# Kernel tuning notes

Hardware: AMD Instinct MI355X
Metric: run time of the kernel (lower is better)

Reference implementation:

```python
import jax, jax.numpy as jnp
import numpy as np

D_MODEL = 1024
N_HEADS = 16
HEAD_DIM = D_MODEL // N_HEADS
WINDOW = 256


def setup_inputs() -> dict:
    key = jax.random.key(0)
    ks = jax.random.split(key, 5)
    s = 1.0 / np.sqrt(D_MODEL)
    x = jax.random.normal(ks[0], (1, 4096, D_MODEL), dtype=jnp.float32)
    W_qkv = jax.random.uniform(ks[1], (D_MODEL, 3 * D_MODEL), jnp.float32, -s, s)
    b_qkv = jax.random.uniform(ks[2], (3 * D_MODEL,), jnp.float32, -s, s)
    W_proj = jax.random.uniform(ks[3], (D_MODEL, D_MODEL), jnp.float32, -s, s)
    b_proj = jax.random.uniform(ks[4], (D_MODEL,), jnp.float32, -s, s)
    return {"x": x, "W_qkv": W_qkv, "b_qkv": b_qkv, "W_proj": W_proj, "b_proj": b_proj}


def reference(x, W_qkv, b_qkv, W_proj, b_proj):
    b, t, c = x.shape
    qkv = x @ W_qkv + b_qkv  # [b,t,3c]
    q, k, v = jnp.split(qkv, 3, axis=-1)
    # [b,h,t,d]
    q = q.reshape(b, t, N_HEADS, HEAD_DIM).transpose(0, 2, 1, 3)
    k = k.reshape(b, t, N_HEADS, HEAD_DIM).transpose(0, 2, 1, 3)
    v = v.reshape(b, t, N_HEADS, HEAD_DIM).transpose(0, 2, 1, 3)
    att = jnp.einsum('bhqd,bhkd->bhqk', q, k) / np.sqrt(HEAD_DIM)
    idx = jnp.arange(t)
    diff = idx[:, None] - idx[None, :]  # query - key
    allowed = (diff >= 0) & (diff < WINDOW)  # causal & local window
    att = jnp.where(allowed[None, None], att, -jnp.inf)
    att = jax.nn.softmax(att, axis=-1)
    y = jnp.einsum('bhqk,bhkd->bhqd', att, v)
    y = y.transpose(0, 2, 1, 3).reshape(b, t, c)
    return y @ W_proj + b_proj
```

## Files before the change

### kernel.cpp

```cpp
#include <hip/hip_runtime.h>
#include <stdint.h>

#define TSEQ 4096
#define DMODEL 1024
#define N3 3072
#define NHEADS 16
#define HDIM 64
#define WINDOW 256

typedef __attribute__((ext_vector_type(8))) short short8;
typedef __attribute__((ext_vector_type(4))) float f32x4;

__device__ __forceinline__ unsigned short f2bf(float f) {
  unsigned u = __builtin_bit_cast(unsigned, f);
  return (unsigned short)((u + 0x7fffu + ((u >> 16) & 1u)) >> 16);
}

__device__ __forceinline__ unsigned cvtpk(float lo, float hi) {
  unsigned r;
  asm("v_cvt_pk_bf16_f32 %0, %1, %2" : "=v"(r) : "v"(lo), "v"(hi));
  return r;
}

__device__ __forceinline__ f32x4 mfma16(short8 a, short8 b, f32x4 c) {
  return __builtin_amdgcn_mfma_f32_16x16x32_bf16(a, b, c, 0, 0, 0);
}

__device__ __forceinline__ void g2lds16(const void* g, void* l) {
  __builtin_amdgcn_global_load_lds(
      (const __attribute__((address_space(1))) void*)(uintptr_t)g,
      (__attribute__((address_space(3))) void*)(uintptr_t)l,
      16, 0, 0);
}


__global__ __launch_bounds__(256) void cvt_f32_bf16_v4(const float* __restrict__ in,
                                                       unsigned short* __restrict__ out) {
  int i = (blockIdx.x * 256 + threadIdx.x) * 4;
  float4 v = *(const float4*)(in + i);
  unsigned lo = cvtpk(v.x, v.y), hi = cvtpk(v.z, v.w);
  unsigned long long packed = (unsigned long long)lo | ((unsigned long long)hi << 32);
  *(unsigned long long*)(out + i) = packed;
}

__global__ __launch_bounds__(256) void transpose_cvt2(const float* __restrict__ Wqkv,
                                                      const float* __restrict__ Wproj,
                                                      unsigned short* __restrict__ oQkvT,
                                                      unsigned short* __restrict__ oProjT) {
  __shared__ float tile[32][33];
  int bx = blockIdx.x;
  const float* in;
  unsigned short* out;
  int C;
  if (bx < 96) {
    in = Wqkv; out = oQkvT; C = N3;
  } else {
    bx -= 96; in = Wproj; out = oProjT; C = DMODEL;
  }
  const int R = DMODEL;
  int c0 = bx * 32;
  int r0 = blockIdx.y * 32;
  int tx = threadIdx.x, ty = threadIdx.y;
#pragma unroll
  for (int i = 0; i < 32; i += 8)
    tile[ty + i][tx] = in[(size_t)(r0 + ty + i) * C + c0 + tx];
  __syncthreads();
#pragma unroll
  for (int i = 0; i < 32; i += 8)
    out[(size_t)(c0 + ty + i) * R + r0 + tx] = f2bf(tile[tx][ty + i]);
}


template <int EPI>
__global__ __launch_bounds__(256)
void gemm_bf16_128(const unsigned short* __restrict__ A,
                   const unsigned short* __restrict__ BT,
                   const float* __restrict__ bias,
                   unsigned short* __restrict__ oQ,
                   unsigned short* __restrict__ oK,
                   unsigned short* __restrict__ oVT,
                   float* __restrict__ oF) {
  __shared__ unsigned short Asm[2][128 * 32];
  __shared__ unsigned short Bsm[2][128 * 32];
  const int K = 1024;
  int m0 = blockIdx.x * 128;
  int n0 = blockIdx.y * 128;
  int tid = threadIdx.x;
  int w = tid >> 6, lane = tid & 63;
  int l15 = lane & 15, l4 = lane >> 4;
  int wm = (w >> 1) * 64, wn = (w & 1) * 64;

  f32x4 acc[4][4];
#pragma unroll
  for (int i = 0; i < 4; i++)
#pragma unroll
    for (int j = 0; j < 4; j++) acc[i][j] = (f32x4){0.f, 0.f, 0.f, 0.f};

  int lr = lane >> 2;
  int slot = ((lane & 3) * 16) ^ (((lr >> 1) & 3) << 4);
  const char* aG = (const char*)(A + (size_t)(m0 + w * 32 + lr) * K) + slot;
  const char* bG = (const char*)(BT + (size_t)(n0 + w * 32 + lr) * K) + slot;
  const size_t rowSkip = (size_t)16 * K * 2;

  auto stage = [&](int s, int b) {
    int koff = s * 64;
    g2lds16(aG + koff, &Asm[b][w * 1024]);
    g2lds16(aG + rowSkip + koff, &Asm[b][w * 1024 + 512]);
    g2lds16(bG + koff, &Bsm[b][w * 1024]);
    g2lds16(bG + rowSkip + koff, &Bsm[b][w * 1024 + 512]);
  };

  int sX = ((l15 >> 1) & 3) << 4;

  auto compute = [&](int b) {
    short8 af[4], bfr[4];
#pragma unroll
    for (int mi = 0; mi < 4; mi++) {
      int rA = wm + mi * 16 + l15;
      af[mi] = *(const short8*)((const char*)Asm[b] + rA * 64 + ((l4 * 16) ^ sX));
    }
#pragma unroll
    for (int ni = 0; ni < 4; ni++) {
      int rB = wn + ni * 16 + l15;
      bfr[ni] = *(const short8*)((const char*)Bsm[b] + rB * 64 + ((l4 * 16) ^ sX));
    }
#pragma unroll
    for (int mi = 0; mi < 4; mi++)
#pragma unroll
      for (int ni = 0; ni < 4; ni++)
        acc[mi][ni] = mfma16(af[mi], bfr[ni], acc[mi][ni]);
  };

  const int NS = K / 32;
  stage(0, 0);
  for (int s = 0; s < NS; s++) {
    if (s + 1 < NS) {
      stage(s + 1, (s + 1) & 1);
      asm volatile("s_waitcnt vmcnt(4)" ::: "memory");
    } else {
      asm volatile("s_waitcnt vmcnt(0)" ::: "memory");
    }
    __builtin_amdgcn_s_barrier();
    __builtin_amdgcn_sched_barrier(0);
    compute(s & 1);
    __builtin_amdgcn_sched_barrier(0);
    __builtin_amdgcn_s_barrier();
  }

#pragma unroll
  for (int ni = 0; ni < 4; ni++) {
    int nn = n0 + wn + ni * 16 + l15;
    float bv = bias[nn];
    int c = nn & 1023;
    int hh = c >> 6, dd = c & 63;
#pragma unroll
    for (int mi = 0; mi < 4; mi++) {
      int mm = m0 + wm + mi * 16 + l4 * 4;
      float v0 = acc[mi][ni][0] + bv;
      float v1 = acc[mi][ni][1] + bv;
      float v2 = acc[mi][ni][2] + bv;
      float v3 = acc[mi][ni][3] + bv;
      if (EPI == 1) {
        oF[(size_t)(mm + 0) * 1024 + nn] = v0;
        oF[(size_t)(mm + 1) * 1024 + nn] = v1;
        oF[(size_t)(mm + 2) * 1024 + nn] = v2;
        oF[(size_t)(mm + 3) * 1024 + nn] = v3;
      } else if (nn < 1024) {
        oQ[((size_t)hh * TSEQ + mm + 0) * 64 + dd] = f2bf(v0 * 0.125f);
        oQ[((size_t)hh * TSEQ + mm + 1) * 64 + dd] = f2bf(v1 * 0.125f);
        oQ[((size_t)hh * TSEQ + mm + 2) * 64 + dd] = f2bf(v2 * 0.125f);
        oQ[((size_t)hh * TSEQ + mm + 3) * 64 + dd] = f2bf(v3 * 0.125f);
      } else if (nn < 2048) {
        oK[((size_t)hh * TSEQ + mm + 0) * 64 + dd] = f2bf(v0);
        oK[((size_t)hh * TSEQ + mm + 1) * 64 + dd] = f2bf(v1);
        oK[((size_t)hh * TSEQ + mm + 2) * 64 + dd] = f2bf(v2);
        oK[((size_t)hh * TSEQ + mm + 3) * 64 + dd] = f2bf(v3);
      } else {
        unsigned lo = cvtpk(v0, v1), hi = cvtpk(v2, v3);
        unsigned long long pv = (unsigned long long)lo | ((unsigned long long)hi << 32);
        *(unsigned long long*)(oVT + ((size_t)hh * 64 + dd) * TSEQ + mm) = pv;
      }
    }
  }
}


__global__ __launch_bounds__(256)
void attn_swa(const unsigned short* __restrict__ Qa,
              const unsigned short* __restrict__ Ka,
              const unsigned short* __restrict__ Vt,
              unsigned short* __restrict__ Y) {
  __shared__ __align__(16) char KV[2][16384];
  __shared__ __align__(16) unsigned char Pl[4][2048];
  int flat = blockIdx.x;
  int swz = (flat & 7) * 128 + (flat >> 3);
  int h = swz >> 6, qb = swz & 63;
  int w = threadIdx.x >> 6, lane = threadIdx.x & 63;
  int l15 = lane & 15, l4 = lane >> 4;
  int qrow0 = qb * 64 + w * 16;
  int q = qrow0 + l15;

  const unsigned short* qp = Qa + ((size_t)h * TSEQ + q) * 64 + l4 * 8;
  short8 qf0 = *(const short8*)qp;
  short8 qf1 = *(const short8*)(qp + 32);

  const char* kgb = (const char*)(Ka + (size_t)h * TSEQ * 64);
  const char* vgb = (const char*)(Vt + (size_t)h * 64 * TSEQ);

  auto stage = [&](int kt, int b) {
    int kbase = kt * 64;
    int sub = lane >> 3, slot = (lane & 7) * 16;
    if (w < 2) {
      int R0 = w * 32;
      const char* src = kgb + (size_t)kbase * 128;
#pragma unroll
      for (int j = 0; j < 4; j++) {
        int r = R0 + j * 8 + sub;
        g2lds16(src + r * 128 + (slot ^ ((r & 7) << 4)), &KV[b][R0 * 128 + j * 1024]);
      }
    } else {
      int D0 = (w - 2) * 32;
      const char* src = vgb + (size_t)kbase * 2;
#pragma unroll
      for (int j = 0; j < 4; j++) {
        int d = D0 + j * 8 + sub;
        g2lds16(src + (size_t)d * 8192 + (slot ^ ((d & 7) << 4)),
                &KV[b][8192 + D0 * 128 + j * 1024]);
      }
    }
  };

  float m = -1e30f, lsum = 0.f;
  f32x4 o[4];
#pragma unroll
  for (int ni = 0; ni < 4; ni++) o[ni] = (f32x4){0.f, 0.f, 0.f, 0.f};

  unsigned char* pw = Pl[w];
  int xw = (l15 & 7) << 4;

  auto compute = [&](int kt, int b, int MODE) {
    int kbase = kt * 64;
    const char* kb = KV[b];
    const char* vb = KV[b] + 8192;
    f32x4 s[4];
#pragma unroll
    for (int ni = 0; ni < 4; ni++) {
      int rb = (ni * 16 + l15) * 128;
      short8 k0 = *(const short8*)(kb + rb + ((l4 * 16) ^ xw));
      short8 k1 = *(const short8*)(kb + rb + ((64 + l4 * 16) ^ xw));
      f32x4 z = (f32x4){0.f, 0.f, 0.f, 0.f};
      z = mfma16(k0, qf0, z);
      s[ni] = mfma16(k1, qf1, z);
    }
    if (MODE != 0) {
#pragma unroll
      for (int ni = 0; ni < 4; ni++)
#pragma unroll
        for (int r = 0; r < 4; r++) {
          int key = kbase + ni * 16 + l4 * 4 + r;
          bool ok = (MODE == 2) ? (key <= q) : (q - key < WINDOW);
          s[ni][r] = ok ? s[ni][r] : -1e30f;
        }
    }
    float pm0 = fmaxf(fmaxf(s[0][0], s[0][1]), fmaxf(s[0][2], s[0][3]));
    float pm1 = fmaxf(fmaxf(s[1][0], s[1][1]), fmaxf(s[1][2], s[1][3]));
    float pm2 = fmaxf(fmaxf(s[2][0], s[2][1]), fmaxf(s[2][2], s[2][3]));
    float pm3 = fmaxf(fmaxf(s[3][0], s[3][1]), fmaxf(s[3][2], s[3][3]));
    float pm = fmaxf(fmaxf(pm0, pm1), fmaxf(pm2, pm3));
    pm = fmaxf(pm, __shfl_xor(pm, 16, 64));
    pm = fmaxf(pm, __shfl_xor(pm, 32, 64));
    float mn = fmaxf(m, pm);
    float alpha = __expf(m - mn);
    m = mn;
    float rs = 0.f;
#pragma unroll
    for (int ni = 0; ni < 4; ni++)
#pragma unroll
      for (int r = 0; r < 4; r++) {
        float p = __expf(s[ni][r] - mn);
        s[ni][r] = p;
        rs += p;
      }
    rs += __shfl_xor(rs, 16, 64);
    rs += __shfl_xor(rs, 32, 64);
    lsum = lsum * alpha + rs;
#pragma unroll
    for (int ni = 0; ni < 4; ni++) {
      unsigned lo = cvtpk(s[ni][0], s[ni][1]);
      unsigned hi = cvtpk(s[ni][2], s[ni][3]);
      unsigned long long pv = (unsigned long long)lo | ((unsigned long long)hi << 32);
      *(unsigned long long*)(pw + l15 * 128 + ((ni * 32 + l4 * 8) ^ xw)) = pv;
    }
    short8 pa0 = *(const short8*)(pw + l15 * 128 + ((l4 * 16) ^ xw));
    short8 pa1 = *(const short8*)(pw + l15 * 128 + ((64 + l4 * 16) ^ xw));
#pragma unroll
    for (int ni = 0; ni < 4; ni++)
#pragma unroll
      for (int r = 0; r < 4; r++) o[ni][r] *= alpha;
#pragma unroll
    for (int ni = 0; ni < 4; ni++) {
      int rb = (ni * 16 + l15) * 128;
      short8 v0 = *(const short8*)(vb + rb + ((l4 * 16) ^ xw));
      short8 v1 = *(const short8*)(vb + rb + ((64 + l4 * 16) ^ xw));
      o[ni] = mfma16(v0, pa0, o[ni]);
      o[ni] = mfma16(v1, pa1, o[ni]);
    }
  };

  int kt0 = qb >= 4 ? qb - 4 : 0;
  int NT = qb - kt0 + 1;
  stage(kt0, 0);
  for (int t = 0; t < NT; t++) {
    int kt = kt0 + t;
    if (t + 1 < NT) {
      stage(kt + 1, (t + 1) & 1);
      asm volatile("s_waitcnt vmcnt(4)" ::: "memory");
    } else {
      asm volatile("s_waitcnt vmcnt(0)" ::: "memory");
    }
    __builtin_amdgcn_s_barrier();
    __builtin_amdgcn_sched_barrier(0);
    int MODE = (t == NT - 1) ? 2 : ((qb >= 4 && t == 0) ? 1 : 0);
    compute(kt, t & 1, MODE);
    __builtin_amdgcn_sched_barrier(0);
    __builtin_amdgcn_s_barrier();
  }

  float inv = 1.f / lsum;
#pragma unroll
  for (int ni = 0; ni < 4; ni++) {
    unsigned lo = cvtpk(o[ni][0] * inv, o[ni][1] * inv);
    unsigned hi = cvtpk(o[ni][2] * inv, o[ni][3] * inv);
    unsigned long long yv = (unsigned long long)lo | ((unsigned long long)hi << 32);
    *(unsigned long long*)(Y + (size_t)q * DMODEL + h * 64 + ni * 16 + l4 * 4) = yv;
  }
}


extern "C" void kernel_launch(void* const* d_in, const int* in_sizes, int n_in,
                              void* d_out, int out_size, void* d_ws, size_t ws_size,
                              hipStream_t stream) {
  const float* x = (const float*)d_in[0];
  const float* Wqkv = (const float*)d_in[1];
  const float* bqkv = (const float*)d_in[2];
  const float* Wproj = (const float*)d_in[3];
  const float* bproj = (const float*)d_in[4];
  float* out = (float*)d_out;

  unsigned short* ws = (unsigned short*)d_ws;
  unsigned short* xb = ws;
  unsigned short* wqkvT = xb + (size_t)TSEQ * DMODEL;
  unsigned short* wprojT = wqkvT + (size_t)N3 * DMODEL;
  unsigned short* qarr = wprojT + (size_t)DMODEL * DMODEL;
  unsigned short* karr = qarr + (size_t)NHEADS * TSEQ * HDIM;
  unsigned short* vtarr = karr + (size_t)NHEADS * TSEQ * HDIM;
  unsigned short* yarr = vtarr + (size_t)NHEADS * TSEQ * HDIM;

  cvt_f32_bf16_v4<<<(TSEQ * DMODEL) / 1024, 256, 0, stream>>>(x, xb);
  transpose_cvt2<<<dim3(128, 32), dim3(32, 8), 0, stream>>>(Wqkv, Wproj, wqkvT, wprojT);
  gemm_bf16_128<0><<<dim3(TSEQ / 128, N3 / 128), 256, 0, stream>>>(xb, wqkvT, bqkv, qarr, karr, vtarr, nullptr);
  attn_swa<<<1024, 256, 0, stream>>>(qarr, karr, vtarr, yarr);
  gemm_bf16_128<1><<<dim3(TSEQ / 128, DMODEL / 128), 256, 0, stream>>>(yarr, wprojT, bproj, nullptr, nullptr, nullptr, out);
}
```

Measured before the change: 85.55 us.

## Merge prep kernels and shrink GEMM tiles for more workgroups

Fuses the x-to-bf16 conversion and the weight transpose/convert into a single launch, removing one kernel launch. Templates the GEMM on tile shape, using 128x64 tiles for the QKV projection and 64x64 tiles for the output projection. This raises the workgroup count so the 256 CUs are better filled, especially for the small output GEMM, which had only 256 blocks. The cost is less data reuse per tile, more global traffic per FLOP, and smaller per-wave MFMA batches.

```diff
diff --git a/kernel.cpp b/kernel.cpp
--- a/kernel.cpp
+++ b/kernel.cpp
@@ -34,21 +34,25 @@
 }
 
 
-__global__ __launch_bounds__(256) void cvt_f32_bf16_v4(const float* __restrict__ in,
-                                                       unsigned short* __restrict__ out) {
-  int i = (blockIdx.x * 256 + threadIdx.x) * 4;
-  float4 v = *(const float4*)(in + i);
-  unsigned lo = cvtpk(v.x, v.y), hi = cvtpk(v.z, v.w);
-  unsigned long long packed = (unsigned long long)lo | ((unsigned long long)hi << 32);
-  *(unsigned long long*)(out + i) = packed;
-}
-
-__global__ __launch_bounds__(256) void transpose_cvt2(const float* __restrict__ Wqkv,
-                                                      const float* __restrict__ Wproj,
-                                                      unsigned short* __restrict__ oQkvT,
-                                                      unsigned short* __restrict__ oProjT) {
+__global__ __launch_bounds__(256) void prep(const float* __restrict__ x,
+                                            const float* __restrict__ Wqkv,
+                                            const float* __restrict__ Wproj,
+                                            unsigned short* __restrict__ xb,
+                                            unsigned short* __restrict__ oQkvT,
+                                            unsigned short* __restrict__ oProjT) {
   __shared__ float tile[32][33];
-  int bx = blockIdx.x;
+  int b = blockIdx.x;
+  int tid = threadIdx.x;
+  if (b < 4096) {
+    int i = (b * 256 + tid) * 4;
+    float4 v = *(const float4*)(x + i);
+    unsigned lo = cvtpk(v.x, v.y), hi = cvtpk(v.z, v.w);
+    unsigned long long packed = (unsigned long long)lo | ((unsigned long long)hi << 32);
+    *(unsigned long long*)(xb + i) = packed;
+    return;
+  }
+  b -= 4096;
+  int bx = b & 127, by = b >> 7;
   const float* in;
   unsigned short* out;
   int C;
@@ -59,8 +63,8 @@
   }
   const int R = DMODEL;
   int c0 = bx * 32;
-  int r0 = blockIdx.y * 32;
-  int tx = threadIdx.x, ty = threadIdx.y;
+  int r0 = by * 32;
+  int tx = tid & 31, ty = tid >> 5;
 #pragma unroll
   for (int i = 0; i < 32; i += 8)
     tile[ty + i][tx] = in[(size_t)(r0 + ty + i) * C + c0 + tx];
@@ -71,72 +75,79 @@
 }
 
 
-template <int EPI>
+template <int EPI, int MI, int NI>
 __global__ __launch_bounds__(256)
-void gemm_bf16_128(const unsigned short* __restrict__ A,
-                   const unsigned short* __restrict__ BT,
-                   const float* __restrict__ bias,
-                   unsigned short* __restrict__ oQ,
-                   unsigned short* __restrict__ oK,
-                   unsigned short* __restrict__ oVT,
-                   float* __restrict__ oF) {
-  __shared__ unsigned short Asm[2][128 * 32];
-  __shared__ unsigned short Bsm[2][128 * 32];
+void gemm_bf16(const unsigned short* __restrict__ A,
+               const unsigned short* __restrict__ BT,
+               const float* __restrict__ bias,
+               unsigned short* __restrict__ oQ,
+               unsigned short* __restrict__ oK,
+               unsigned short* __restrict__ oVT,
+               float* __restrict__ oF) {
+  constexpr int BM = MI * 32, BN = NI * 32;
+  constexpr int LPS = MI / 2 + NI / 2;
+  __shared__ unsigned short Asm[2][BM * 32];
+  __shared__ unsigned short Bsm[2][BN * 32];
   const int K = 1024;
-  int m0 = blockIdx.x * 128;
-  int n0 = blockIdx.y * 128;
+  int m0 = blockIdx.x * BM;
+  int n0 = blockIdx.y * BN;
   int tid = threadIdx.x;
   int w = tid >> 6, lane = tid & 63;
   int l15 = lane & 15, l4 = lane >> 4;
-  int wm = (w >> 1) * 64, wn = (w & 1) * 64;
-
-  f32x4 acc[4][4];
-#pragma unroll
-  for (int i = 0; i < 4; i++)
-#pragma unroll
-    for (int j = 0; j < 4; j++) acc[i][j] = (f32x4){0.f, 0.f, 0.f, 0.f};
+  int wm = (w >> 1) * (MI * 16), wn = (w & 1) * (NI * 16);
+
+  f32x4 acc[MI][NI];
+#pragma unroll
+  for (int i = 0; i < MI; i++)
+#pragma unroll
+    for (int j = 0; j < NI; j++) acc[i][j] = (f32x4){0.f, 0.f, 0.f, 0.f};
 
   int lr = lane >> 2;
   int slot = ((lane & 3) * 16) ^ (((lr >> 1) & 3) << 4);
-  const char* aG = (const char*)(A + (size_t)(m0 + w * 32 + lr) * K) + slot;
-  const char* bG = (const char*)(BT + (size_t)(n0 + w * 32 + lr) * K) + slot;
+  const char* aG = (const char*)(A + (size_t)(m0 + w * (BM / 4) + lr) * K) + slot;
+  const char* bG = (const char*)(BT + (size_t)(n0 + w * (BN / 4) + lr) * K) + slot;
   const size_t rowSkip = (size_t)16 * K * 2;
 
   auto stage = [&](int s, int b) {
     int koff = s * 64;
-    g2lds16(aG + koff, &Asm[b][w * 1024]);
-    g2lds16(aG + rowSkip + koff, &Asm[b][w * 1024 + 512]);
-    g2lds16(bG + koff, &Bsm[b][w * 1024]);
-    g2lds16(bG + rowSkip + koff, &Bsm[b][w * 1024 + 512]);
+#pragma unroll
+    for (int j = 0; j < MI / 2; j++)
+      g2lds16(aG + j * rowSkip + koff, &Asm[b][(w * (MI / 2) + j) * 512]);
+#pragma unroll
+    for (int j = 0; j < NI / 2; j++)
+      g2lds16(bG + j * rowSkip + koff, &Bsm[b][(w * (NI / 2) + j) * 512]);
   };
 
   int sX = ((l15 >> 1) & 3) << 4;
 
   auto compute = [&](int b) {
-    short8 af[4], bfr[4];
-#pragma unroll
-    for (int mi = 0; mi < 4; mi++) {
+    short8 af[MI], bfr[NI];
+#pragma unroll
+    for (int mi = 0; mi < MI; mi++) {
       int rA = wm + mi * 16 + l15;
       af[mi] = *(const short8*)((const char*)Asm[b] + rA * 64 + ((l4 * 16) ^ sX));
     }
 #pragma unroll
-    for (int ni = 0; ni < 4; ni++) {
+    for (int ni = 0; ni < NI; ni++) {
       int rB = wn + ni * 16 + l15;
       bfr[ni] = *(const short8*)((const char*)Bsm[b] + rB * 64 + ((l4 * 16) ^ sX));
     }
 #pragma unroll
-    for (int mi = 0; mi < 4; mi++)
-#pragma unroll
-      for (int ni = 0; ni < 4; ni++)
+    for (int mi = 0; mi < MI; mi++)
+#pragma unroll
+      for (int ni = 0; ni < NI; ni++)
         acc[mi][ni] = mfma16(af[mi], bfr[ni], acc[mi][ni]);
   };
 
   const int NS = K / 32;
   stage(0, 0);
+#pragma unroll 1
   for (int s = 0; s < NS; s++) {
     if (s + 1 < NS) {
       stage(s + 1, (s + 1) & 1);
-      asm volatile("s_waitcnt vmcnt(4)" ::: "memory");
+      if constexpr (LPS == 3) asm volatile("s_waitcnt vmcnt(3)" ::: "memory");
+      else if constexpr (LPS == 2) asm volatile("s_waitcnt vmcnt(2)" ::: "memory");
+      else asm volatile("s_waitcnt vmcnt(4)" ::: "memory");
     } else {
       asm volatile("s_waitcnt vmcnt(0)" ::: "memory");
     }
@@ -148,13 +159,13 @@
   }
 
 #pragma unroll
-  for (int ni = 0; ni < 4; ni++) {
+  for (int ni = 0; ni < NI; ni++) {
     int nn = n0 + wn + ni * 16 + l15;
     float bv = bias[nn];
     int c = nn & 1023;
     int hh = c >> 6, dd = c & 63;
 #pragma unroll
-    for (int mi = 0; mi < 4; mi++) {
+    for (int mi = 0; mi < MI; mi++) {
       int mm = m0 + wm + mi * 16 + l4 * 4;
       float v0 = acc[mi][ni][0] + bv;
       float v1 = acc[mi][ni][1] + bv;
@@ -356,9 +367,8 @@
   unsigned short* vtarr = karr + (size_t)NHEADS * TSEQ * HDIM;
   unsigned short* yarr = vtarr + (size_t)NHEADS * TSEQ * HDIM;
 
-  cvt_f32_bf16_v4<<<(TSEQ * DMODEL) / 1024, 256, 0, stream>>>(x, xb);
-  transpose_cvt2<<<dim3(128, 32), dim3(32, 8), 0, stream>>>(Wqkv, Wproj, wqkvT, wprojT);
-  gemm_bf16_128<0><<<dim3(TSEQ / 128, N3 / 128), 256, 0, stream>>>(xb, wqkvT, bqkv, qarr, karr, vtarr, nullptr);
+  prep<<<8192, 256, 0, stream>>>(x, Wqkv, Wproj, xb, wqkvT, wprojT);
+  gemm_bf16<0, 4, 2><<<dim3(TSEQ / 128, N3 / 64), 256, 0, stream>>>(xb, wqkvT, bqkv, qarr, karr, vtarr, nullptr);
   attn_swa<<<1024, 256, 0, stream>>>(qarr, karr, vtarr, yarr);
-  gemm_bf16_128<1><<<dim3(TSEQ / 128, DMODEL / 128), 256, 0, stream>>>(yarr, wprojT, bproj, nullptr, nullptr, nullptr, out);
-}
+  gemm_bf16<1, 2, 2><<<dim3(TSEQ / 64, DMODEL / 64), 256, 0, stream>>>(yarr, wprojT, bproj, nullptr, nullptr, nullptr, out);
+}
```

Result: slower. 93.00 us (+8.7%).
